# Optimization experiments

Measured on AMD Instinct MI355X. Metric: run time of the kernel, lower is better.

## Reference

```python
import jax, jax.numpy as jnp
import numpy as np

LN_EPS = 1e-5
START_TOKEN = 0  # voc['<s>']

V, E = 512, 512
H = 2 * E            # 1024
B, T = 256, 128


def setup_inputs() -> dict:
    key = jax.random.key(0)
    ks = jax.random.split(key, 12)
    s = lambda *shape: 0.05  # small init scale
    return {
        "target": jax.random.randint(ks[0], (B, T), 0, V),
        "emb": jax.random.normal(ks[1], (V, E), jnp.float32) * 0.05,
        "projW": jax.random.normal(ks[2], (H, E), jnp.float32) * 0.05,
        "projb": jnp.zeros((H,), jnp.float32),
        "gru_Wih": jax.random.normal(ks[3], (3, 3 * H, H), jnp.float32) * 0.03,
        "gru_Whh": jax.random.normal(ks[4], (3, 3 * H, H), jnp.float32) * 0.03,
        "gru_bih": jnp.zeros((3, 3 * H), jnp.float32),
        "gru_bhh": jnp.zeros((3, 3 * H), jnp.float32),
        "ln_s": jnp.ones((3, H), jnp.float32),
        "ln_b": jnp.zeros((3, H), jnp.float32),
        "fc1W": jax.random.normal(ks[5], (2 * H, H), jnp.float32) * 0.03,
        "fc1b": jnp.zeros((2 * H,), jnp.float32),
        "fc2W": jax.random.normal(ks[6], (V, 2 * H), jnp.float32) * 0.03,
        "fc2b": jnp.zeros((V,), jnp.float32),
    }


def _layernorm(x, scale, bias):
    mu = jnp.mean(x, axis=-1, keepdims=True)
    var = jnp.mean(jnp.square(x - mu), axis=-1, keepdims=True)
    return (x - mu) * jax.lax.rsqrt(var + LN_EPS) * scale + bias


def _gru_cell(x, h, Wih, Whh, bih, bhh):
    # PyTorch GRUCell: gates stacked [r; z; n] along dim 0 of [3H, H] weights
    gi = x @ Wih.T + bih      # [B, 3H]
    gh = h @ Whh.T + bhh      # [B, 3H]
    i_r, i_z, i_n = jnp.split(gi, 3, axis=-1)
    h_r, h_z, h_n = jnp.split(gh, 3, axis=-1)
    r = jax.nn.sigmoid(i_r + h_r)
    z = jax.nn.sigmoid(i_z + h_z)
    n = jnp.tanh(i_n + r * h_n)
    return (1.0 - z) * n + z * h


def reference(target, emb, projW, projb, gru_Wih, gru_Whh, gru_bih, gru_bhh,
              ln_s, ln_b, fc1W, fc1b, fc2W, fc2b):
    # teacher-forced likelihood: x_t = [<s>, target_0, ..., target_{T-2}]
    bsz = target.shape[0]
    start = jnp.full((bsz, 1), START_TOKEN, dtype=target.dtype)
    x_in = jnp.concatenate([start, target[:, :-1]], axis=1)   # [B, T]

    def step(carry, xs):
        h, acc = carry                 # h: [3, B, H]
        tok, tgt = xs                  # [B], [B]
        x = emb[tok]                   # [B, E]  embedding gather
        x = x @ projW.T + projb        # [B, H]  (dropout = identity in eval)
        new_h = []
        for i in range(3):             # three structurally distinct cells
            hi = _gru_cell(x, h[i], gru_Wih[i], gru_Whh[i], gru_bih[i], gru_bhh[i])
            hi = _layernorm(hi + x, ln_s[i], ln_b[i])
            new_h.append(hi)
            x = hi
        logits = jax.nn.relu(x @ fc1W.T + fc1b) @ fc2W.T + fc2b   # [B, V]
        lp = jax.nn.log_softmax(logits, axis=-1)
        acc = acc + jnp.take_along_axis(lp, tgt[:, None], axis=1)[:, 0]
        return (jnp.stack(new_h, axis=0), acc), None

    h0 = jnp.zeros((3, bsz, projW.shape[0]), dtype=projW.dtype)
    acc0 = jnp.zeros((bsz,), dtype=projW.dtype)
    (_, log_probs), _ = jax.lax.scan(step, (h0, acc0), (x_in.T, target.T))
    return log_probs
```

## Files before the change

kernel.cpp:

```cpp
#include <hip/hip_runtime.h>
#include <stdint.h>

#define HID   1024
#define B3H   3072
#define BSZ   256
#define TLEN  128
#define VOC   512
#define EMB   512
#define SLAB  ((size_t)BSZ * B3H)

typedef unsigned short u16;
typedef short bf16x8 __attribute__((ext_vector_type(8)));
typedef float f32x4  __attribute__((ext_vector_type(4)));

__device__ __forceinline__ float bf2f(u16 u) {
    union { float f; uint32_t i; } c; c.i = ((uint32_t)u) << 16; return c.f;
}
__device__ __forceinline__ u16 f2bf(float f) {
    union { float f; uint32_t i; } c; c.f = f;
    uint32_t u = c.i;
    return (u16)((u + 0x7FFFu + ((u >> 16) & 1u)) >> 16);
}
__device__ __forceinline__ float sigm(float x)  { return 1.f / (1.f + __expf(-x)); }
__device__ __forceinline__ float tanhf_(float x) {
    float e = __expf(-2.f * fabsf(x));
    float r = (1.f - e) / (1.f + e);
    return x < 0.f ? -r : r;
}

__device__ __forceinline__ void gll16(const u16* g, u16* l) {
    __builtin_amdgcn_global_load_lds(
        (__attribute__((address_space(1))) void*)(u16*)g,
        (__attribute__((address_space(3))) void*)l, 16, 0, 0);
}

__device__ __forceinline__ void stage_tile(const u16* __restrict__ src, int ld,
                                           u16* __restrict__ lds, int wid, int lane) {
#pragma unroll
    for (int i = 0; i < 2; i++) {
        int row16 = wid * 2 + i;
        const u16* g = src + (size_t)(row16 * 16 + (lane >> 2)) * ld + (lane & 3) * 8;
        u16* l = lds + row16 * 16 * 32;
        gll16(g, l);
    }
}
__device__ __forceinline__ void stage_tile64(const u16* __restrict__ src, int ld,
                                             u16* __restrict__ lds, int wid, int lane) {
    const u16* g = src + (size_t)(wid * 16 + (lane >> 2)) * ld + (lane & 3) * 8;
    gll16(g, lds + wid * 16 * 32);
}

template<int KTOT>
__device__ __forceinline__ void gemm_tiles(const u16* __restrict__ A, const u16* __restrict__ W,
                                           f32x4 acc[4][4], int wid, int lane) {
    __shared__ u16 As[2][128 * 32], Ws[2][128 * 32];
    const int r = lane & 15, g8 = (lane >> 4) * 8;
    const int mq = wid & 1, nq = wid >> 1;
    int buf = 0;
    stage_tile(A, KTOT, As[0], wid, lane);
    stage_tile(W, KTOT, Ws[0], wid, lane);
    __syncthreads();
    for (int k0 = 0; k0 < KTOT; k0 += 32) {
        if (k0 + 32 < KTOT) {
            stage_tile(A + k0 + 32, KTOT, As[buf ^ 1], wid, lane);
            stage_tile(W + k0 + 32, KTOT, Ws[buf ^ 1], wid, lane);
        }
        bf16x8 a[4], b[4];
#pragma unroll
        for (int i = 0; i < 4; i++) a[i] = *(const bf16x8*)(As[buf] + (mq * 64 + i * 16 + r) * 32 + g8);
#pragma unroll
        for (int i = 0; i < 4; i++) b[i] = *(const bf16x8*)(Ws[buf] + (nq * 64 + i * 16 + r) * 32 + g8);
#pragma unroll
        for (int mi = 0; mi < 4; mi++)
#pragma unroll
            for (int ni = 0; ni < 4; ni++)
                acc[mi][ni] = __builtin_amdgcn_mfma_f32_16x16x32_bf16(a[mi], b[ni], acc[mi][ni], 0, 0, 0);
        __syncthreads();
        buf ^= 1;
    }
}

template<int KTOT>
__device__ __forceinline__ void gemm_tiles64(const u16* __restrict__ A, const u16* __restrict__ W,
                                             f32x4 acc[2][4], int wid, int lane) {
    __shared__ u16 As[2][64 * 32], Ws[2][128 * 32];
    const int r = lane & 15, g8 = (lane >> 4) * 8;
    const int mq = wid & 1, nq = wid >> 1;
    int buf = 0;
    stage_tile64(A, KTOT, As[0], wid, lane);
    stage_tile(W, KTOT, Ws[0], wid, lane);
    __syncthreads();
    for (int k0 = 0; k0 < KTOT; k0 += 32) {
        if (k0 + 32 < KTOT) {
            stage_tile64(A + k0 + 32, KTOT, As[buf ^ 1], wid, lane);
            stage_tile(W + k0 + 32, KTOT, Ws[buf ^ 1], wid, lane);
        }
        bf16x8 a[2], b[4];
#pragma unroll
        for (int i = 0; i < 2; i++) a[i] = *(const bf16x8*)(As[buf] + (mq * 32 + i * 16 + r) * 32 + g8);
#pragma unroll
        for (int i = 0; i < 4; i++) b[i] = *(const bf16x8*)(Ws[buf] + (nq * 64 + i * 16 + r) * 32 + g8);
#pragma unroll
        for (int mi = 0; mi < 2; mi++)
#pragma unroll
            for (int ni = 0; ni < 4; ni++)
                acc[mi][ni] = __builtin_amdgcn_mfma_f32_16x16x32_bf16(a[mi], b[ni], acc[mi][ni], 0, 0, 0);
        __syncthreads();
        buf ^= 1;
    }
}

__global__ void k_convert(const float* __restrict__ in, u16* __restrict__ out, int n) {
    int i = (blockIdx.x * 256 + threadIdx.x) * 4;
    if (i >= n) return;
    float4 f = *(const float4*)(in + i);
    uint32_t lo = (uint32_t)f2bf(f.x) | ((uint32_t)f2bf(f.y) << 16);
    uint32_t hi = (uint32_t)f2bf(f.z) | ((uint32_t)f2bf(f.w) << 16);
    uint2 p; p.x = lo; p.y = hi;
    *(uint2*)(out + i) = p;
}

__global__ void __launch_bounds__(256) k_proj_s(const u16* __restrict__ emb_bf, const u16* __restrict__ projW_bf,
                        const float* __restrict__ projb, const int* __restrict__ target,
                        u16* __restrict__ X_all) {
    int nt = blockIdx.x, mt = blockIdx.y;
    int wid = threadIdx.x >> 6, lane = threadIdx.x & 63;
    __shared__ u16 As[2][128 * 32], Ws[2][128 * 32];
    const u16* arow[2];
#pragma unroll
    for (int i = 0; i < 2; i++) {
        int lr = (wid * 2 + i) * 16 + (lane >> 2);
        int gr = mt * 128 + lr;
        int t = gr >> 8, b = gr & 255;
        int tok = (t == 0) ? 0 : target[b * TLEN + t - 1];
        arow[i] = emb_bf + (size_t)tok * EMB + (lane & 3) * 8;
    }
    const u16* W = projW_bf + (size_t)(nt * 128) * EMB;
    const int r = lane & 15, g8 = (lane >> 4) * 8;
    const int mq = wid & 1, nq = wid >> 1;
    f32x4 acc[4][4] = {};
    int buf = 0;
#pragma unroll
    for (int i = 0; i < 2; i++) gll16(arow[i], As[0] + (wid * 2 + i) * 512);
    stage_tile(W, EMB, Ws[0], wid, lane);
    __syncthreads();
    for (int k0 = 0; k0 < EMB; k0 += 32) {
        if (k0 + 32 < EMB) {
#pragma unroll
            for (int i = 0; i < 2; i++) gll16(arow[i] + k0 + 32, As[buf ^ 1] + (wid * 2 + i) * 512);
            stage_tile(W + k0 + 32, EMB, Ws[buf ^ 1], wid, lane);
        }
        bf16x8 a[4], b[4];
#pragma unroll
        for (int i = 0; i < 4; i++) a[i] = *(const bf16x8*)(As[buf] + (mq * 64 + i * 16 + r) * 32 + g8);
#pragma unroll
        for (int i = 0; i < 4; i++) b[i] = *(const bf16x8*)(Ws[buf] + (nq * 64 + i * 16 + r) * 32 + g8);
#pragma unroll
        for (int mi = 0; mi < 4; mi++)
#pragma unroll
            for (int ni = 0; ni < 4; ni++)
                acc[mi][ni] = __builtin_amdgcn_mfma_f32_16x16x32_bf16(a[mi], b[ni], acc[mi][ni], 0, 0, 0);
        __syncthreads();
        buf ^= 1;
    }
    int c = lane & 15, r0 = (lane >> 4) * 4;
#pragma unroll
    for (int mi = 0; mi < 4; mi++)
#pragma unroll
        for (int e = 0; e < 4; e++) {
            size_t row = (size_t)(mt * 128 + mq * 64 + mi * 16 + r0 + e);
#pragma unroll
            for (int ni = 0; ni < 4; ni++) {
                int col = nt * 128 + nq * 64 + ni * 16 + c;
                X_all[row * HID + col] = f2bf(acc[mi][ni][e] + projb[col]);
            }
        }
}

__global__ void __launch_bounds__(256) k_gstep(int wv,
    const u16* __restrict__ X_all, const u16* __restrict__ h_bf,
    const u16* __restrict__ Wih, const u16* __restrict__ Whh,
    float* __restrict__ giP, float* __restrict__ ghP) {
    int bid = blockIdx.x;
    int g = bid / 48, rem = bid % 48, mt = rem / 24, nt = rem % 24;
    int cell = g % 3; bool isgh = (g >= 3);
    int t = wv - cell;
    if (t < 0 || t >= TLEN) return;
    int rd = (wv + 1) & 1;
    const u16* A;
    if (isgh)            A = h_bf + (size_t)(rd * 3 + cell)     * BSZ * HID;
    else if (cell == 0)  A = X_all + (size_t)t * BSZ * HID;
    else                 A = h_bf + (size_t)(rd * 3 + cell - 1) * BSZ * HID;
    A += (size_t)(mt * 128) * HID;
    const u16* W = (isgh ? Whh : Wih) + (size_t)cell * B3H * HID + (size_t)(nt * 128) * HID;
    float*     C = (isgh ? ghP : giP) + (size_t)cell * SLAB + (size_t)(mt * 128) * B3H + nt * 128;

    int wid = threadIdx.x >> 6, lane = threadIdx.x & 63;
    f32x4 acc[4][4] = {};
    gemm_tiles<HID>(A, W, acc, wid, lane);
    int mq = wid & 1, nq = wid >> 1;
    int c = lane & 15, r0 = (lane >> 4) * 4;
#pragma unroll
    for (int mi = 0; mi < 4; mi++)
#pragma unroll
        for (int e = 0; e < 4; e++) {
            float* Cw = C + (size_t)(mq * 64 + mi * 16 + r0 + e) * B3H;
#pragma unroll
            for (int ni = 0; ni < 4; ni++)
                __builtin_nontemporal_store(acc[mi][ni][e], Cw + nq * 64 + ni * 16 + c);
        }
}

template<int KTOT, int EPI>
__global__ void __launch_bounds__(256) k_gemm_s(const u16* __restrict__ A, const u16* __restrict__ W,
                                                const float* __restrict__ bias, void* __restrict__ Cout, int ldc) {
    int nt = blockIdx.x, mt = blockIdx.y;
    int wid = threadIdx.x >> 6, lane = threadIdx.x & 63;
    f32x4 acc[4][4] = {};
    gemm_tiles<KTOT>(A + (size_t)(mt * 128) * KTOT, W + (size_t)(nt * 128) * KTOT, acc, wid, lane);
    int mq = wid & 1, nq = wid >> 1;
    int c = lane & 15, r0 = (lane >> 4) * 4;
#pragma unroll
    for (int mi = 0; mi < 4; mi++)
#pragma unroll
        for (int e = 0; e < 4; e++) {
            size_t row = (size_t)(mt * 128 + mq * 64 + mi * 16 + r0 + e);
#pragma unroll
            for (int ni = 0; ni < 4; ni++) {
                int col = nt * 128 + nq * 64 + ni * 16 + c;
                float x = acc[mi][ni][e] + bias[col];
                if (EPI == 1) ((u16*)Cout)[row * ldc + col] = f2bf(fmaxf(x, 0.f));
                else          ((float*)Cout)[row * ldc + col] = x;
            }
        }
}

template<int KTOT>
__global__ void __launch_bounds__(256) k_gemm_s64(const u16* __restrict__ A, const u16* __restrict__ W,
                                                  const float* __restrict__ bias, float* __restrict__ Cout, int ldc) {
    int nt = blockIdx.x, mt = blockIdx.y;
    int wid = threadIdx.x >> 6, lane = threadIdx.x & 63;
    f32x4 acc[2][4] = {};
    gemm_tiles64<KTOT>(A + (size_t)(mt * 64) * KTOT, W + (size_t)(nt * 128) * KTOT, acc, wid, lane);
    int mq = wid & 1, nq = wid >> 1;
    int c = lane & 15, r0 = (lane >> 4) * 4;
#pragma unroll
    for (int mi = 0; mi < 2; mi++)
#pragma unroll
        for (int e = 0; e < 4; e++) {
            size_t row = (size_t)(mt * 64 + mq * 32 + mi * 16 + r0 + e);
#pragma unroll
            for (int ni = 0; ni < 4; ni++) {
                int col = nt * 128 + nq * 64 + ni * 16 + c;
                Cout[row * ldc + col] = acc[mi][ni][e] + bias[col];
            }
        }
}

__global__ void __launch_bounds__(256) k_wew(int wv,
    const float* __restrict__ giP, const float* __restrict__ ghP,
    const float* __restrict__ bih_all, const float* __restrict__ bhh_all,
    float* __restrict__ h_f32, u16* __restrict__ h_bf, u16* __restrict__ X_all,
    const float* __restrict__ ln_s_all, const float* __restrict__ ln_b_all) {
    int cell = blockIdx.y;
    int t = wv - cell;
    if (t < 0 || t >= TLEN) return;
    int wid = threadIdx.x >> 6, lane = threadIdx.x & 63;
    int b = blockIdx.x * 4 + wid;
    int rd = (wv + 1) & 1, wr = wv & 1;

    const float* gi  = giP + (size_t)cell * SLAB + (size_t)b * B3H;
    const float* gh  = ghP + (size_t)cell * SLAB + (size_t)b * B3H;
    const float* bih = bih_all + cell * B3H;
    const float* bhh = bhh_all + cell * B3H;
    const float* lns = ln_s_all + cell * HID;
    const float* lnb = ln_b_all + cell * HID;
    const float* hprev = h_f32 + ((size_t)(rd * 3 + cell) * BSZ + b) * HID;
    float*       hout  = h_f32 + ((size_t)(wr * 3 + cell) * BSZ + b) * HID;
    u16*         hbout = h_bf  + ((size_t)(wr * 3 + cell) * BSZ + b) * HID;
    const float* xsrcf = (cell > 0) ? h_f32 + ((size_t)(rd * 3 + cell - 1) * BSZ + b) * HID : nullptr;
    const u16*   xsrcb = X_all + ((size_t)t * BSZ + b) * HID;

    float val[16], s = 0.f, s2 = 0.f;
#pragma unroll
    for (int e = 0; e < 4; e++) {
        int j = e * 256 + lane * 4;
        float gg[3][4], hh[3][4];
#pragma unroll
        for (int g = 0; g < 3; g++) {
            int o = g * HID + j;
            f32x4 a = __builtin_nontemporal_load((const f32x4*)(gi + o));
            float4 ab = *(const float4*)(bih + o);
            gg[g][0] = a[0] + ab.x; gg[g][1] = a[1] + ab.y; gg[g][2] = a[2] + ab.z; gg[g][3] = a[3] + ab.w;
            f32x4 h4 = __builtin_nontemporal_load((const f32x4*)(gh + o));
            float4 hb = *(const float4*)(bhh + o);
            hh[g][0] = h4[0] + hb.x; hh[g][1] = h4[1] + hb.y; hh[g][2] = h4[2] + hb.z; hh[g][3] = h4[3] + hb.w;
        }
        float4 hp = *(const float4*)(hprev + j);
        float hpv[4] = {hp.x, hp.y, hp.z, hp.w};
        float xv[4];
        if (cell == 0) {
            ushort4 u = *(const ushort4*)(xsrcb + j);
            xv[0] = bf2f(u.x); xv[1] = bf2f(u.y); xv[2] = bf2f(u.z); xv[3] = bf2f(u.w);
        } else {
            float4 x4 = *(const float4*)(xsrcf + j);
            xv[0] = x4.x; xv[1] = x4.y; xv[2] = x4.z; xv[3] = x4.w;
        }
#pragma unroll
        for (int q = 0; q < 4; q++) {
            float r = sigm(gg[0][q] + hh[0][q]);
            float z = sigm(gg[1][q] + hh[1][q]);
            float n = tanhf_(gg[2][q] + r * hh[2][q]);
            float v = (1.f - z) * n + z * hpv[q] + xv[q];
            val[e * 4 + q] = v; s += v; s2 += v * v;
        }
    }
#pragma unroll
    for (int o = 32; o > 0; o >>= 1) { s += __shfl_xor(s, o); s2 += __shfl_xor(s2, o); }
    float mu = s * (1.f / HID);
    float inv = rsqrtf(s2 * (1.f / HID) - mu * mu + 1e-5f);
#pragma unroll
    for (int e = 0; e < 4; e++) {
        int j = e * 256 + lane * 4;
        float4 sc = *(const float4*)(lns + j);
        float4 bi = *(const float4*)(lnb + j);
        float o0 = (val[e * 4 + 0] - mu) * inv * sc.x + bi.x;
        float o1 = (val[e * 4 + 1] - mu) * inv * sc.y + bi.y;
        float o2 = (val[e * 4 + 2] - mu) * inv * sc.z + bi.z;
        float o3 = (val[e * 4 + 3] - mu) * inv * sc.w + bi.w;
        float4 of; of.x = o0; of.y = o1; of.z = o2; of.w = o3;
        *(float4*)(hout + j) = of;
        u16 b0 = f2bf(o0), b1 = f2bf(o1), b2 = f2bf(o2), b3 = f2bf(o3);
        uint64_t packed = (uint64_t)b0 | ((uint64_t)b1 << 16) | ((uint64_t)b2 << 32) | ((uint64_t)b3 << 48);
        *(uint64_t*)(hbout + j) = packed;
        if (cell == 2) {
            __builtin_nontemporal_store(packed, (uint64_t*)(X_all + ((size_t)t * BSZ + b) * HID + j));
        }
    }
}

__global__ void __launch_bounds__(256) k_lse2(const float* __restrict__ part, const int* __restrict__ target,
                       int c0, float* __restrict__ LP) {
    int wid = threadIdx.x >> 6, lane = threadIdx.x & 63;
    int r = blockIdx.x * 4 + wid;
    const float* row = part + (size_t)r * VOC;
    float v[8];
#pragma unroll
    for (int e = 0; e < 8; e++) v[e] = row[e * 64 + lane];
    float m = v[0];
#pragma unroll
    for (int e = 1; e < 8; e++) m = fmaxf(m, v[e]);
    for (int o = 32; o > 0; o >>= 1) m = fmaxf(m, __shfl_xor(m, o));
    float s = 0.f;
#pragma unroll
    for (int e = 0; e < 8; e++) s += __expf(v[e] - m);
    for (int o = 32; o > 0; o >>= 1) s += __shfl_xor(s, o);
    int t = c0 + (r >> 8), b = r & 255;
    int tg = target[b * TLEN + t];
    float tv = 0.f;
#pragma unroll
    for (int e = 0; e < 8; e++) if (e * 64 + lane == tg) tv = v[e];
    for (int o = 32; o > 0; o >>= 1) tv += __shfl_xor(tv, o);
    if (lane == 0) LP[(size_t)t * BSZ + b] = tv - (m + logf(s));
}

__global__ void k_out(const float* __restrict__ LP, float* __restrict__ out) {
    int b = threadIdx.x;
    float s = 0.f;
    for (int t = 0; t < TLEN; t++) s += LP[(size_t)t * BSZ + b];
    out[b] = s;
}

extern "C" void kernel_launch(void* const* d_in, const int* in_sizes, int n_in,
                              void* d_out, int out_size, void* d_ws, size_t ws_size,
                              hipStream_t stream) {
    const int*   target = (const int*)  d_in[0];
    const float* emb    = (const float*)d_in[1];
    const float* projW  = (const float*)d_in[2];
    const float* projb  = (const float*)d_in[3];
    const float* gWih   = (const float*)d_in[4];
    const float* gWhh   = (const float*)d_in[5];
    const float* gbih   = (const float*)d_in[6];
    const float* gbhh   = (const float*)d_in[7];
    const float* ln_s   = (const float*)d_in[8];
    const float* ln_b   = (const float*)d_in[9];
    const float* fc1W   = (const float*)d_in[10];
    const float* fc1b   = (const float*)d_in[11];
    const float* fc2W   = (const float*)d_in[12];
    const float* fc2b   = (const float*)d_in[13];
    float* out = (float*)d_out;

    char* ws = (char*)d_ws;
    size_t off = 0;
    auto alloc = [&](size_t bytes) { void* p = ws + off; off += (bytes + 511) & ~511ull; return p; };
    u16* emb_bf   = (u16*)alloc((size_t)VOC * EMB * 2);
    u16* projW_bf = (u16*)alloc((size_t)HID * EMB * 2);
    u16* Wih_bf   = (u16*)alloc((size_t)3 * B3H * HID * 2);
    u16* Whh_bf   = (u16*)alloc((size_t)3 * B3H * HID * 2);
    u16* X_all    = (u16*)alloc((size_t)TLEN * BSZ * HID * 2);
    float* h_f32  = (float*)alloc((size_t)2 * 3 * BSZ * HID * 4);
    u16*   h_bf   = (u16*)alloc((size_t)2 * 3 * BSZ * HID * 2);
    float* LP     = (float*)alloc((size_t)TLEN * BSZ * 4);
    float* giP    = (float*)alloc(3 * SLAB * 4);
    float* ghP    = (float*)alloc(3 * SLAB * 4);
    if (off > ws_size) return;

    u16*   fc1W_bf = (u16*)giP;
    u16*   fc2W_bf = (u16*)((char*)giP + (size_t)2048 * HID * 2);
    u16*   a1c     = (u16*)ghP;
    float* partc   = (float*)h_f32;

    auto cvt = [&](const float* s, u16* d, int n) {
        k_convert<<<dim3((n / 4 + 255) / 256), 256, 0, stream>>>(s, d, n);
    };
    cvt(emb,   emb_bf,   VOC * EMB);
    cvt(projW, projW_bf, HID * EMB);
    cvt(gWih,  Wih_bf,   3 * B3H * HID);
    cvt(gWhh,  Whh_bf,   3 * B3H * HID);
    (void)hipMemsetAsync(h_f32, 0, (size_t)2 * 3 * BSZ * HID * 4, stream);
    (void)hipMemsetAsync(h_bf,  0, (size_t)2 * 3 * BSZ * HID * 2, stream);

    k_proj_s<<<dim3(HID / 128, (TLEN * BSZ) / 128), 256, 0, stream>>>(emb_bf, projW_bf, projb, target, X_all);

    for (int wv = 0; wv < TLEN + 2; wv++) {
        k_gstep<<<dim3(288), 256, 0, stream>>>(wv, X_all, h_bf, Wih_bf, Whh_bf, giP, ghP);
        k_wew<<<dim3(BSZ / 4, 3), 256, 0, stream>>>(wv, giP, ghP, gbih, gbhh, h_f32, h_bf, X_all, ln_s, ln_b);
    }

    cvt(fc1W, fc1W_bf, 2048 * HID);
    cvt(fc2W, fc2W_bf, VOC * 2048);
    const int CH = 8;
    for (int c0 = 0; c0 < TLEN; c0 += CH) {
        int M = CH * BSZ;
        const u16* Ain = X_all + (size_t)c0 * BSZ * HID;
        k_gemm_s<HID, 1><<<dim3(2048 / 128, M / 128), 256, 0, stream>>>(Ain, fc1W_bf, fc1b, a1c, 2048);
        k_gemm_s64<2048><<<dim3(VOC / 128, M / 64), 256, 0, stream>>>(a1c, fc2W_bf, fc2b, partc, VOC);
        k_lse2<<<dim3(M / 4), 256, 0, stream>>>(partc, target, c0, LP);
    }
    k_out<<<1, 256, 0, stream>>>(LP, out);
}
```

Before: 4.949 ms.

## Move cell-0 input GEMM into elementwise kernel and use swizzled K=64 GEMM core

Cell 0's input-gate GEMM for step t+1 now runs inside the elementwise kernel of step t, with extra blocks, and writes into a double-buffered gi0 slab. This shortens the per-wave gstep kernel from 288 to 240 blocks and overlaps that GEMM with the elementwise work. A one-off GEMM computes gi0 for the first timestep. The recurrent GEMMs switch to a new core with 64-wide K tiles and an XOR-swizzled LDS layout, meant to cut LDS bank conflicts and halve loop and barrier overhead. The cost is more LDS per block, which may lower occupancy, and a mix of heavy GEMM blocks and light elementwise blocks in one launch.

```diff
diff --git a/kernel.cpp b/kernel.cpp
--- a/kernel.cpp
+++ b/kernel.cpp
@@ -40,16 +40,9 @@
     for (int i = 0; i < 2; i++) {
         int row16 = wid * 2 + i;
         const u16* g = src + (size_t)(row16 * 16 + (lane >> 2)) * ld + (lane & 3) * 8;
-        u16* l = lds + row16 * 16 * 32;
-        gll16(g, l);
-    }
-}
-__device__ __forceinline__ void stage_tile64(const u16* __restrict__ src, int ld,
-                                             u16* __restrict__ lds, int wid, int lane) {
-    const u16* g = src + (size_t)(wid * 16 + (lane >> 2)) * ld + (lane & 3) * 8;
-    gll16(g, lds + wid * 16 * 32);
-}
-
+        gll16(g, lds + row16 * 16 * 32);
+    }
+}
 template<int KTOT>
 __device__ __forceinline__ void gemm_tiles(const u16* __restrict__ A, const u16* __restrict__ W,
                                            f32x4 acc[4][4], int wid, int lane) {
@@ -80,31 +73,52 @@
     }
 }
 
+__device__ __forceinline__ void stage64(const u16* __restrict__ src, int ld,
+                                        u16* __restrict__ lds, int wid, int lane) {
+    int rl = lane >> 3;
+    int chunk = (lane & 7) ^ rl;
+#pragma unroll
+    for (int i = 0; i < 4; i++) {
+        int row = wid * 32 + i * 8 + rl;
+        gll16(src + (size_t)row * ld + chunk * 8, lds + (wid * 32 + i * 8) * 64);
+    }
+}
+__device__ __forceinline__ bf16x8 lds_rd64(const u16* base, int row, int cc) {
+    return *(const bf16x8*)(base + row * 64 + ((cc ^ (row & 7)) * 8));
+}
 template<int KTOT>
-__device__ __forceinline__ void gemm_tiles64(const u16* __restrict__ A, const u16* __restrict__ W,
-                                             f32x4 acc[2][4], int wid, int lane) {
-    __shared__ u16 As[2][64 * 32], Ws[2][128 * 32];
-    const int r = lane & 15, g8 = (lane >> 4) * 8;
+__device__ __forceinline__ void gemm_core64(const u16* __restrict__ A, const u16* __restrict__ W,
+                                            f32x4 acc[4][4], int wid, int lane) {
+    __shared__ u16 As[2][128 * 64], Ws[2][128 * 64];
+    const int r = lane & 15, cc0 = lane >> 4;
     const int mq = wid & 1, nq = wid >> 1;
     int buf = 0;
-    stage_tile64(A, KTOT, As[0], wid, lane);
-    stage_tile(W, KTOT, Ws[0], wid, lane);
+    stage64(A, KTOT, As[0], wid, lane);
+    stage64(W, KTOT, Ws[0], wid, lane);
     __syncthreads();
-    for (int k0 = 0; k0 < KTOT; k0 += 32) {
-        if (k0 + 32 < KTOT) {
-            stage_tile64(A + k0 + 32, KTOT, As[buf ^ 1], wid, lane);
-            stage_tile(W + k0 + 32, KTOT, Ws[buf ^ 1], wid, lane);
-        }
-        bf16x8 a[2], b[4];
-#pragma unroll
-        for (int i = 0; i < 2; i++) a[i] = *(const bf16x8*)(As[buf] + (mq * 32 + i * 16 + r) * 32 + g8);
-#pragma unroll
-        for (int i = 0; i < 4; i++) b[i] = *(const bf16x8*)(Ws[buf] + (nq * 64 + i * 16 + r) * 32 + g8);
-#pragma unroll
-        for (int mi = 0; mi < 2; mi++)
+    for (int k0 = 0; k0 < KTOT; k0 += 64) {
+        if (k0 + 64 < KTOT) {
+            stage64(A + k0 + 64, KTOT, As[buf ^ 1], wid, lane);
+            stage64(W + k0 + 64, KTOT, Ws[buf ^ 1], wid, lane);
+        }
+        bf16x8 a0[4], b0[4], a1[4], b1[4];
+#pragma unroll
+        for (int i = 0; i < 4; i++) {
+            a0[i] = lds_rd64(As[buf], mq * 64 + i * 16 + r, cc0);
+            a1[i] = lds_rd64(As[buf], mq * 64 + i * 16 + r, cc0 + 4);
+            b0[i] = lds_rd64(Ws[buf], nq * 64 + i * 16 + r, cc0);
+            b1[i] = lds_rd64(Ws[buf], nq * 64 + i * 16 + r, cc0 + 4);
+        }
+#pragma unroll
+        for (int mi = 0; mi < 4; mi++)
 #pragma unroll
             for (int ni = 0; ni < 4; ni++)
-                acc[mi][ni] = __builtin_amdgcn_mfma_f32_16x16x32_bf16(a[mi], b[ni], acc[mi][ni], 0, 0, 0);
+                acc[mi][ni] = __builtin_amdgcn_mfma_f32_16x16x32_bf16(a0[mi], b0[ni], acc[mi][ni], 0, 0, 0);
+#pragma unroll
+        for (int mi = 0; mi < 4; mi++)
+#pragma unroll
+            for (int ni = 0; ni < 4; ni++)
+                acc[mi][ni] = __builtin_amdgcn_mfma_f32_16x16x32_bf16(a1[mi], b1[ni], acc[mi][ni], 0, 0, 0);
         __syncthreads();
         buf ^= 1;
     }
@@ -178,26 +192,26 @@
 }
 
 __global__ void __launch_bounds__(256) k_gstep(int wv,
-    const u16* __restrict__ X_all, const u16* __restrict__ h_bf,
+    const u16* __restrict__ h_bf,
     const u16* __restrict__ Wih, const u16* __restrict__ Whh,
     float* __restrict__ giP, float* __restrict__ ghP) {
     int bid = blockIdx.x;
     int g = bid / 48, rem = bid % 48, mt = rem / 24, nt = rem % 24;
-    int cell = g % 3; bool isgh = (g >= 3);
+    int cell; bool isgh;
+    if (g < 2) { cell = g + 1; isgh = false; } else { cell = g - 2; isgh = true; }
     int t = wv - cell;
     if (t < 0 || t >= TLEN) return;
     int rd = (wv + 1) & 1;
-    const u16* A;
-    if (isgh)            A = h_bf + (size_t)(rd * 3 + cell)     * BSZ * HID;
-    else if (cell == 0)  A = X_all + (size_t)t * BSZ * HID;
-    else                 A = h_bf + (size_t)(rd * 3 + cell - 1) * BSZ * HID;
+    const u16* A = isgh ? h_bf + (size_t)(rd * 3 + cell) * BSZ * HID
+                        : h_bf + (size_t)(rd * 3 + cell - 1) * BSZ * HID;
     A += (size_t)(mt * 128) * HID;
     const u16* W = (isgh ? Whh : Wih) + (size_t)cell * B3H * HID + (size_t)(nt * 128) * HID;
-    float*     C = (isgh ? ghP : giP) + (size_t)cell * SLAB + (size_t)(mt * 128) * B3H + nt * 128;
+    float*     C = (isgh ? ghP + (size_t)cell * SLAB : giP + (size_t)(cell - 1) * SLAB)
+                   + (size_t)(mt * 128) * B3H + nt * 128;
 
     int wid = threadIdx.x >> 6, lane = threadIdx.x & 63;
     f32x4 acc[4][4] = {};
-    gemm_tiles<HID>(A, W, acc, wid, lane);
+    gemm_core64<HID>(A, W, acc, wid, lane);
     int mq = wid & 1, nq = wid >> 1;
     int c = lane & 15, r0 = (lane >> 4) * 4;
 #pragma unroll
@@ -211,65 +225,48 @@
         }
 }
 
-template<int KTOT, int EPI>
-__global__ void __launch_bounds__(256) k_gemm_s(const u16* __restrict__ A, const u16* __restrict__ W,
-                                                const float* __restrict__ bias, void* __restrict__ Cout, int ldc) {
-    int nt = blockIdx.x, mt = blockIdx.y;
-    int wid = threadIdx.x >> 6, lane = threadIdx.x & 63;
-    f32x4 acc[4][4] = {};
-    gemm_tiles<KTOT>(A + (size_t)(mt * 128) * KTOT, W + (size_t)(nt * 128) * KTOT, acc, wid, lane);
-    int mq = wid & 1, nq = wid >> 1;
-    int c = lane & 15, r0 = (lane >> 4) * 4;
-#pragma unroll
-    for (int mi = 0; mi < 4; mi++)
-#pragma unroll
-        for (int e = 0; e < 4; e++) {
-            size_t row = (size_t)(mt * 128 + mq * 64 + mi * 16 + r0 + e);
-#pragma unroll
-            for (int ni = 0; ni < 4; ni++) {
-                int col = nt * 128 + nq * 64 + ni * 16 + c;
-                float x = acc[mi][ni][e] + bias[col];
-                if (EPI == 1) ((u16*)Cout)[row * ldc + col] = f2bf(fmaxf(x, 0.f));
-                else          ((float*)Cout)[row * ldc + col] = x;
-            }
-        }
-}
-
-template<int KTOT>
-__global__ void __launch_bounds__(256) k_gemm_s64(const u16* __restrict__ A, const u16* __restrict__ W,
-                                                  const float* __restrict__ bias, float* __restrict__ Cout, int ldc) {
-    int nt = blockIdx.x, mt = blockIdx.y;
-    int wid = threadIdx.x >> 6, lane = threadIdx.x & 63;
-    f32x4 acc[2][4] = {};
-    gemm_tiles64<KTOT>(A + (size_t)(mt * 64) * KTOT, W + (size_t)(nt * 128) * KTOT, acc, wid, lane);
-    int mq = wid & 1, nq = wid >> 1;
-    int c = lane & 15, r0 = (lane >> 4) * 4;
-#pragma unroll
-    for (int mi = 0; mi < 2; mi++)
-#pragma unroll
-        for (int e = 0; e < 4; e++) {
-            size_t row = (size_t)(mt * 64 + mq * 32 + mi * 16 + r0 + e);
-#pragma unroll
-            for (int ni = 0; ni < 4; ni++) {
-                int col = nt * 128 + nq * 64 + ni * 16 + c;
-                Cout[row * ldc + col] = acc[mi][ni][e] + bias[col];
-            }
-        }
-}
-
-__global__ void __launch_bounds__(256) k_wew(int wv,
+__global__ void __launch_bounds__(256) k_ewgi(int wv,
+    u16* __restrict__ X_all,
+    const float* __restrict__ gi0P_all, float* __restrict__ gi0P_wr_base,
     const float* __restrict__ giP, const float* __restrict__ ghP,
     const float* __restrict__ bih_all, const float* __restrict__ bhh_all,
-    float* __restrict__ h_f32, u16* __restrict__ h_bf, u16* __restrict__ X_all,
-    const float* __restrict__ ln_s_all, const float* __restrict__ ln_b_all) {
-    int cell = blockIdx.y;
+    float* __restrict__ h_f32, u16* __restrict__ h_bf,
+    const float* __restrict__ ln_s_all, const float* __restrict__ ln_b_all,
+    const u16* __restrict__ Wih0) {
+    int bid = blockIdx.x;
+    int wid = threadIdx.x >> 6, lane = threadIdx.x & 63;
+
+    if (bid >= 192) {
+        int t1 = wv + 1;
+        if (t1 >= TLEN) return;
+        int j = bid - 192, mt = j / 24, nt = j % 24;
+        const u16* A = X_all + (size_t)t1 * BSZ * HID + (size_t)(mt * 128) * HID;
+        const u16* W = Wih0 + (size_t)(nt * 128) * HID;
+        float* C = gi0P_wr_base + (size_t)(t1 & 1) * SLAB + (size_t)(mt * 128) * B3H + nt * 128;
+        f32x4 acc[4][4] = {};
+        gemm_core64<HID>(A, W, acc, wid, lane);
+        int mq = wid & 1, nq = wid >> 1;
+        int c = lane & 15, r0 = (lane >> 4) * 4;
+#pragma unroll
+        for (int mi = 0; mi < 4; mi++)
+#pragma unroll
+            for (int e = 0; e < 4; e++) {
+                float* Cw = C + (size_t)(mq * 64 + mi * 16 + r0 + e) * B3H;
+#pragma unroll
+                for (int ni = 0; ni < 4; ni++)
+                    __builtin_nontemporal_store(acc[mi][ni][e], Cw + nq * 64 + ni * 16 + c);
+            }
+        return;
+    }
+
+    int cell = bid >> 6;
     int t = wv - cell;
     if (t < 0 || t >= TLEN) return;
-    int wid = threadIdx.x >> 6, lane = threadIdx.x & 63;
-    int b = blockIdx.x * 4 + wid;
+    int b = (bid & 63) * 4 + wid;
     int rd = (wv + 1) & 1, wr = wv & 1;
 
-    const float* gi  = giP + (size_t)cell * SLAB + (size_t)b * B3H;
+    const float* gi = (cell == 0) ? gi0P_all + (size_t)(t & 1) * SLAB + (size_t)b * B3H
+                                  : giP + (size_t)(cell - 1) * SLAB + (size_t)b * B3H;
     const float* gh  = ghP + (size_t)cell * SLAB + (size_t)b * B3H;
     const float* bih = bih_all + cell * B3H;
     const float* bhh = bhh_all + cell * B3H;
@@ -337,6 +334,83 @@
             __builtin_nontemporal_store(packed, (uint64_t*)(X_all + ((size_t)t * BSZ + b) * HID + j));
         }
     }
+}
+
+template<int KTOT, int EPI>
+__global__ void __launch_bounds__(256) k_gemm_s(const u16* __restrict__ A, const u16* __restrict__ W,
+                                                const float* __restrict__ bias, void* __restrict__ Cout, int ldc) {
+    int nt = blockIdx.x, mt = blockIdx.y;
+    int wid = threadIdx.x >> 6, lane = threadIdx.x & 63;
+    f32x4 acc[4][4] = {};
+    gemm_tiles<KTOT>(A + (size_t)(mt * 128) * KTOT, W + (size_t)(nt * 128) * KTOT, acc, wid, lane);
+    int mq = wid & 1, nq = wid >> 1;
+    int c = lane & 15, r0 = (lane >> 4) * 4;
+#pragma unroll
+    for (int mi = 0; mi < 4; mi++)
+#pragma unroll
+        for (int e = 0; e < 4; e++) {
+            size_t row = (size_t)(mt * 128 + mq * 64 + mi * 16 + r0 + e);
+#pragma unroll
+            for (int ni = 0; ni < 4; ni++) {
+                int col = nt * 128 + nq * 64 + ni * 16 + c;
+                float x = acc[mi][ni][e];
+                if (EPI == 0)      ((float*)Cout)[row * ldc + col] = x;
+                else if (EPI == 1) ((u16*)Cout)[row * ldc + col] = f2bf(fmaxf(x + bias[col], 0.f));
+                else               ((float*)Cout)[row * ldc + col] = x + bias[col];
+            }
+        }
+}
+
+__device__ __forceinline__ void stage_tile64r(const u16* __restrict__ src, int ld,
+                                              u16* __restrict__ lds, int wid, int lane) {
+    const u16* g = src + (size_t)(wid * 16 + (lane >> 2)) * ld + (lane & 3) * 8;
+    gll16(g, lds + wid * 16 * 32);
+}
+template<int KTOT>
+__global__ void __launch_bounds__(256) k_gemm_s64(const u16* __restrict__ A, const u16* __restrict__ W,
+                                                  const float* __restrict__ bias, float* __restrict__ Cout, int ldc) {
+    int nt = blockIdx.x, mt = blockIdx.y;
+    int wid = threadIdx.x >> 6, lane = threadIdx.x & 63;
+    __shared__ u16 As[2][64 * 32], Ws[2][128 * 32];
+    const u16* Ab = A + (size_t)(mt * 64) * KTOT;
+    const u16* Wb = W + (size_t)(nt * 128) * KTOT;
+    const int r = lane & 15, g8 = (lane >> 4) * 8;
+    const int mq = wid & 1, nq = wid >> 1;
+    f32x4 acc[2][4] = {};
+    int buf = 0;
+    stage_tile64r(Ab, KTOT, As[0], wid, lane);
+    stage_tile(Wb, KTOT, Ws[0], wid, lane);
+    __syncthreads();
+    for (int k0 = 0; k0 < KTOT; k0 += 32) {
+        if (k0 + 32 < KTOT) {
+            stage_tile64r(Ab + k0 + 32, KTOT, As[buf ^ 1], wid, lane);
+            stage_tile(Wb + k0 + 32, KTOT, Ws[buf ^ 1], wid, lane);
+        }
+        bf16x8 a[2], b[4];
+#pragma unroll
+        for (int i = 0; i < 2; i++) a[i] = *(const bf16x8*)(As[buf] + (mq * 32 + i * 16 + r) * 32 + g8);
+#pragma unroll
+        for (int i = 0; i < 4; i++) b[i] = *(const bf16x8*)(Ws[buf] + (nq * 64 + i * 16 + r) * 32 + g8);
+#pragma unroll
+        for (int mi = 0; mi < 2; mi++)
+#pragma unroll
+            for (int ni = 0; ni < 4; ni++)
+                acc[mi][ni] = __builtin_amdgcn_mfma_f32_16x16x32_bf16(a[mi], b[ni], acc[mi][ni], 0, 0, 0);
+        __syncthreads();
+        buf ^= 1;
+    }
+    int c = lane & 15, r0 = (lane >> 4) * 4;
+#pragma unroll
+    for (int mi = 0; mi < 2; mi++)
+#pragma unroll
+        for (int e = 0; e < 4; e++) {
+            size_t row = (size_t)(mt * 64 + mq * 32 + mi * 16 + r0 + e);
+#pragma unroll
+            for (int ni = 0; ni < 4; ni++) {
+                int col = nt * 128 + nq * 64 + ni * 16 + c;
+                Cout[row * ldc + col] = acc[mi][ni][e] + bias[col];
+            }
+        }
 }
 
 __global__ void __launch_bounds__(256) k_lse2(const float* __restrict__ part, const int* __restrict__ target,
@@ -401,8 +475,9 @@
     float* h_f32  = (float*)alloc((size_t)2 * 3 * BSZ * HID * 4);
     u16*   h_bf   = (u16*)alloc((size_t)2 * 3 * BSZ * HID * 2);
     float* LP     = (float*)alloc((size_t)TLEN * BSZ * 4);
-    float* giP    = (float*)alloc(3 * SLAB * 4);
+    float* giP    = (float*)alloc(2 * SLAB * 4);
     float* ghP    = (float*)alloc(3 * SLAB * 4);
+    float* gi0P   = (float*)alloc(2 * SLAB * 4);
     if (off > ws_size) return;
 
     u16*   fc1W_bf = (u16*)giP;
@@ -421,10 +496,12 @@
     (void)hipMemsetAsync(h_bf,  0, (size_t)2 * 3 * BSZ * HID * 2, stream);
 
     k_proj_s<<<dim3(HID / 128, (TLEN * BSZ) / 128), 256, 0, stream>>>(emb_bf, projW_bf, projb, target, X_all);
+    k_gemm_s<HID, 0><<<dim3(B3H / 128, BSZ / 128), 256, 0, stream>>>(X_all, Wih_bf, nullptr, gi0P, B3H);
 
     for (int wv = 0; wv < TLEN + 2; wv++) {
-        k_gstep<<<dim3(288), 256, 0, stream>>>(wv, X_all, h_bf, Wih_bf, Whh_bf, giP, ghP);
-        k_wew<<<dim3(BSZ / 4, 3), 256, 0, stream>>>(wv, giP, ghP, gbih, gbhh, h_f32, h_bf, X_all, ln_s, ln_b);
+        k_gstep<<<dim3(240), 256, 0, stream>>>(wv, h_bf, Wih_bf, Whh_bf, giP, ghP);
+        k_ewgi<<<dim3(240), 256, 0, stream>>>(wv, X_all, gi0P, gi0P, giP, ghP, gbih, gbhh,
+                                              h_f32, h_bf, ln_s, ln_b, Wih_bf);
     }
 
     cvt(fc1W, fc1W_bf, 2048 * HID);
```

New measurement: 6.433 ms. +30.0%, slower.

## Use full-batch 256x128 tiles in recurrent GRU gate GEMM to halve weight reads

Applied to the files above, without the earlier changes.

The per-wavefront gate GEMM now covers all 256 batch rows per block with a 256x128 tile instead of two 128x128 tiles. Each weight tile is therefore read from global memory once instead of twice, and the grid shrinks from 288 to 144 blocks. Each wave now holds a 4x8 accumulator array, and launch bounds are set to one block per SM. The trade-off is fewer blocks on a 256-CU device, lower occupancy and more register pressure. The 64-row helper is inlined into k_gemm_s64 without functional change.

```diff
diff --git a/kernel.cpp b/kernel.cpp
--- a/kernel.cpp
+++ b/kernel.cpp
@@ -40,14 +40,17 @@
     for (int i = 0; i < 2; i++) {
         int row16 = wid * 2 + i;
         const u16* g = src + (size_t)(row16 * 16 + (lane >> 2)) * ld + (lane & 3) * 8;
-        u16* l = lds + row16 * 16 * 32;
-        gll16(g, l);
-    }
-}
-__device__ __forceinline__ void stage_tile64(const u16* __restrict__ src, int ld,
-                                             u16* __restrict__ lds, int wid, int lane) {
-    const u16* g = src + (size_t)(wid * 16 + (lane >> 2)) * ld + (lane & 3) * 8;
-    gll16(g, lds + wid * 16 * 32);
+        gll16(g, lds + row16 * 16 * 32);
+    }
+}
+__device__ __forceinline__ void stage_tile256(const u16* __restrict__ src, int ld,
+                                              u16* __restrict__ lds, int wid, int lane) {
+#pragma unroll
+    for (int i = 0; i < 4; i++) {
+        int row16 = wid * 4 + i;
+        const u16* g = src + (size_t)(row16 * 16 + (lane >> 2)) * ld + (lane & 3) * 8;
+        gll16(g, lds + row16 * 16 * 32);
+    }
 }
 
 template<int KTOT>
@@ -81,29 +84,28 @@
 }
 
 template<int KTOT>
-__device__ __forceinline__ void gemm_tiles64(const u16* __restrict__ A, const u16* __restrict__ W,
-                                             f32x4 acc[2][4], int wid, int lane) {
-    __shared__ u16 As[2][64 * 32], Ws[2][128 * 32];
+__device__ __forceinline__ void gemm_tiles256(const u16* __restrict__ A, const u16* __restrict__ W,
+                                              f32x4 acc[4][8], int wid, int lane) {
+    __shared__ u16 As[2][256 * 32], Ws[2][128 * 32];
     const int r = lane & 15, g8 = (lane >> 4) * 8;
-    const int mq = wid & 1, nq = wid >> 1;
     int buf = 0;
-    stage_tile64(A, KTOT, As[0], wid, lane);
+    stage_tile256(A, KTOT, As[0], wid, lane);
     stage_tile(W, KTOT, Ws[0], wid, lane);
     __syncthreads();
     for (int k0 = 0; k0 < KTOT; k0 += 32) {
         if (k0 + 32 < KTOT) {
-            stage_tile64(A + k0 + 32, KTOT, As[buf ^ 1], wid, lane);
+            stage_tile256(A + k0 + 32, KTOT, As[buf ^ 1], wid, lane);
             stage_tile(W + k0 + 32, KTOT, Ws[buf ^ 1], wid, lane);
         }
-        bf16x8 a[2], b[4];
-#pragma unroll
-        for (int i = 0; i < 2; i++) a[i] = *(const bf16x8*)(As[buf] + (mq * 32 + i * 16 + r) * 32 + g8);
-#pragma unroll
-        for (int i = 0; i < 4; i++) b[i] = *(const bf16x8*)(Ws[buf] + (nq * 64 + i * 16 + r) * 32 + g8);
-#pragma unroll
-        for (int mi = 0; mi < 2; mi++)
-#pragma unroll
-            for (int ni = 0; ni < 4; ni++)
+        bf16x8 a[4], b[8];
+#pragma unroll
+        for (int i = 0; i < 4; i++) a[i] = *(const bf16x8*)(As[buf] + (wid * 64 + i * 16 + r) * 32 + g8);
+#pragma unroll
+        for (int i = 0; i < 8; i++) b[i] = *(const bf16x8*)(Ws[buf] + (i * 16 + r) * 32 + g8);
+#pragma unroll
+        for (int mi = 0; mi < 4; mi++)
+#pragma unroll
+            for (int ni = 0; ni < 8; ni++)
                 acc[mi][ni] = __builtin_amdgcn_mfma_f32_16x16x32_bf16(a[mi], b[ni], acc[mi][ni], 0, 0, 0);
         __syncthreads();
         buf ^= 1;
@@ -177,12 +179,12 @@
         }
 }
 
-__global__ void __launch_bounds__(256) k_gstep(int wv,
+__global__ void __launch_bounds__(256, 1) k_gstep(int wv,
     const u16* __restrict__ X_all, const u16* __restrict__ h_bf,
     const u16* __restrict__ Wih, const u16* __restrict__ Whh,
     float* __restrict__ giP, float* __restrict__ ghP) {
     int bid = blockIdx.x;
-    int g = bid / 48, rem = bid % 48, mt = rem / 24, nt = rem % 24;
+    int g = bid / 24, nt = bid % 24;
     int cell = g % 3; bool isgh = (g >= 3);
     int t = wv - cell;
     if (t < 0 || t >= TLEN) return;
@@ -191,23 +193,21 @@
     if (isgh)            A = h_bf + (size_t)(rd * 3 + cell)     * BSZ * HID;
     else if (cell == 0)  A = X_all + (size_t)t * BSZ * HID;
     else                 A = h_bf + (size_t)(rd * 3 + cell - 1) * BSZ * HID;
-    A += (size_t)(mt * 128) * HID;
     const u16* W = (isgh ? Whh : Wih) + (size_t)cell * B3H * HID + (size_t)(nt * 128) * HID;
-    float*     C = (isgh ? ghP : giP) + (size_t)cell * SLAB + (size_t)(mt * 128) * B3H + nt * 128;
-
-    int wid = threadIdx.x >> 6, lane = threadIdx.x & 63;
-    f32x4 acc[4][4] = {};
-    gemm_tiles<HID>(A, W, acc, wid, lane);
-    int mq = wid & 1, nq = wid >> 1;
+    float*     C = (isgh ? ghP : giP) + (size_t)cell * SLAB + nt * 128;
+
+    int wid = threadIdx.x >> 6, lane = threadIdx.x & 63;
+    f32x4 acc[4][8] = {};
+    gemm_tiles256<HID>(A, W, acc, wid, lane);
     int c = lane & 15, r0 = (lane >> 4) * 4;
 #pragma unroll
     for (int mi = 0; mi < 4; mi++)
 #pragma unroll
         for (int e = 0; e < 4; e++) {
-            float* Cw = C + (size_t)(mq * 64 + mi * 16 + r0 + e) * B3H;
-#pragma unroll
-            for (int ni = 0; ni < 4; ni++)
-                __builtin_nontemporal_store(acc[mi][ni][e], Cw + nq * 64 + ni * 16 + c);
+            float* Cw = C + (size_t)(wid * 64 + mi * 16 + r0 + e) * B3H;
+#pragma unroll
+            for (int ni = 0; ni < 8; ni++)
+                __builtin_nontemporal_store(acc[mi][ni][e], Cw + ni * 16 + c);
         }
 }
 
@@ -235,14 +235,44 @@
         }
 }
 
+__device__ __forceinline__ void stage_tile64r(const u16* __restrict__ src, int ld,
+                                              u16* __restrict__ lds, int wid, int lane) {
+    const u16* g = src + (size_t)(wid * 16 + (lane >> 2)) * ld + (lane & 3) * 8;
+    gll16(g, lds + wid * 16 * 32);
+}
 template<int KTOT>
 __global__ void __launch_bounds__(256) k_gemm_s64(const u16* __restrict__ A, const u16* __restrict__ W,
                                                   const float* __restrict__ bias, float* __restrict__ Cout, int ldc) {
     int nt = blockIdx.x, mt = blockIdx.y;
     int wid = threadIdx.x >> 6, lane = threadIdx.x & 63;
+    __shared__ u16 As[2][64 * 32], Ws[2][128 * 32];
+    const u16* Ab = A + (size_t)(mt * 64) * KTOT;
+    const u16* Wb = W + (size_t)(nt * 128) * KTOT;
+    const int r = lane & 15, g8 = (lane >> 4) * 8;
+    const int mq = wid & 1, nq = wid >> 1;
     f32x4 acc[2][4] = {};
-    gemm_tiles64<KTOT>(A + (size_t)(mt * 64) * KTOT, W + (size_t)(nt * 128) * KTOT, acc, wid, lane);
-    int mq = wid & 1, nq = wid >> 1;
+    int buf = 0;
+    stage_tile64r(Ab, KTOT, As[0], wid, lane);
+    stage_tile(Wb, KTOT, Ws[0], wid, lane);
+    __syncthreads();
+    for (int k0 = 0; k0 < KTOT; k0 += 32) {
+        if (k0 + 32 < KTOT) {
+            stage_tile64r(Ab + k0 + 32, KTOT, As[buf ^ 1], wid, lane);
+            stage_tile(Wb + k0 + 32, KTOT, Ws[buf ^ 1], wid, lane);
+        }
+        bf16x8 a[2], b[4];
+#pragma unroll
+        for (int i = 0; i < 2; i++) a[i] = *(const bf16x8*)(As[buf] + (mq * 32 + i * 16 + r) * 32 + g8);
+#pragma unroll
+        for (int i = 0; i < 4; i++) b[i] = *(const bf16x8*)(Ws[buf] + (nq * 64 + i * 16 + r) * 32 + g8);
+#pragma unroll
+        for (int mi = 0; mi < 2; mi++)
+#pragma unroll
+            for (int ni = 0; ni < 4; ni++)
+                acc[mi][ni] = __builtin_amdgcn_mfma_f32_16x16x32_bf16(a[mi], b[ni], acc[mi][ni], 0, 0, 0);
+        __syncthreads();
+        buf ^= 1;
+    }
     int c = lane & 15, r0 = (lane >> 4) * 4;
 #pragma unroll
     for (int mi = 0; mi < 2; mi++)
@@ -423,7 +453,7 @@
     k_proj_s<<<dim3(HID / 128, (TLEN * BSZ) / 128), 256, 0, stream>>>(emb_bf, projW_bf, projb, target, X_all);
 
     for (int wv = 0; wv < TLEN + 2; wv++) {
-        k_gstep<<<dim3(288), 256, 0, stream>>>(wv, X_all, h_bf, Wih_bf, Whh_bf, giP, ghP);
+        k_gstep<<<dim3(144), 256, 0, stream>>>(wv, X_all, h_bf, Wih_bf, Whh_bf, giP, ghP);
         k_wew<<<dim3(BSZ / 4, 3), 256, 0, stream>>>(wv, giP, ghP, gbih, gbhh, h_f32, h_bf, X_all, ln_s, ln_b);
     }
 
```

New measurement: 6.596 ms. +33.3%, slower.
